# Kernel tuning notes

Measured on AMD Instinct MI355X. Metric: run time of the kernel, lower is better.

Reference implementation:

```python
import jax, jax.numpy as jnp
import numpy as np

D_MODEL = 1024
N_HEADS = 16
D_K = D_MODEL // N_HEADS
D_FF = 4096
EPS = 1e-5


def layer_norm(x, g, b):
    mu = jnp.mean(x, axis=-1, keepdims=True)
    var = jnp.var(x, axis=-1, keepdims=True)
    return (x - mu) * jax.lax.rsqrt(var + EPS) * g + b


def setup_inputs() -> dict:
    key = jax.random.key(0)
    ks = jax.random.split(key, 16)
    B, S = 4, 2048
    s_in = 1.0 / np.sqrt(D_MODEL)
    s_ff = 1.0 / np.sqrt(D_FF)
    return {
        "x": jax.random.normal(ks[0], (B, S, D_MODEL), jnp.float32),
        "mask": jnp.ones((B, 1, 1, S), jnp.int32),
        "Wq": jax.random.normal(ks[1], (D_MODEL, D_MODEL), jnp.float32) * s_in,
        "bq": jnp.zeros((D_MODEL,), jnp.float32),
        "Wk": jax.random.normal(ks[2], (D_MODEL, D_MODEL), jnp.float32) * s_in,
        "bk": jnp.zeros((D_MODEL,), jnp.float32),
        "Wv": jax.random.normal(ks[3], (D_MODEL, D_MODEL), jnp.float32) * s_in,
        "bv": jnp.zeros((D_MODEL,), jnp.float32),
        "Wo": jax.random.normal(ks[4], (D_MODEL, D_MODEL), jnp.float32) * s_in,
        "bo": jnp.zeros((D_MODEL,), jnp.float32),
        "W1": jax.random.normal(ks[5], (D_MODEL, D_FF), jnp.float32) * s_in,
        "b1": jnp.zeros((D_FF,), jnp.float32),
        "W2": jax.random.normal(ks[6], (D_FF, D_MODEL), jnp.float32) * s_ff,
        "b2": jnp.zeros((D_MODEL,), jnp.float32),
        "ln1_g": jnp.ones((D_MODEL,), jnp.float32),
        "ln1_b": jnp.zeros((D_MODEL,), jnp.float32),
        "ln2_g": jnp.ones((D_MODEL,), jnp.float32),
        "ln2_b": jnp.zeros((D_MODEL,), jnp.float32),
    }


def reference(x, mask, Wq, bq, Wk, bk, Wv, bv, Wo, bo, W1, b1, W2, b2,
              ln1_g, ln1_b, ln2_g, ln2_b):
    B, S, _ = x.shape
    h = layer_norm(x, ln1_g, ln1_b)  # norm1(x), used for q/k/v
    # project and split heads: [B,S,D] -> [B,H,S,Dk]
    def heads(t):
        return t.reshape(B, S, N_HEADS, D_K).transpose(0, 2, 1, 3)
    Q = heads(h @ Wq + bq)
    K = heads(h @ Wk + bk)
    V = heads(h @ Wv + bv)
    scores = jnp.einsum('bhqd,bhkd->bhqk', Q, K) / jnp.sqrt(jnp.float32(D_K))
    scores = jnp.where(mask == 0, jnp.float32(-1e9), scores)
    attn = jax.nn.softmax(scores, axis=-1)
    out = jnp.einsum('bhqk,bhkd->bhqd', attn, V)
    out = out.transpose(0, 2, 1, 3).reshape(B, S, D_MODEL)
    attn_out = out @ Wo + bo
    x = x + attn_out
    # FFN with pre-norm (torch nn.GELU default = exact erf gelu)
    h2 = layer_norm(x, ln2_g, ln2_b)
    ff = jax.nn.gelu(h2 @ W1 + b1, approximate=False) @ W2 + b2
    return x + ff
```

## Files before the change

### kernel.cpp

```cpp
#include <hip/hip_runtime.h>
#include <stdint.h>
#include <string.h>


typedef unsigned int       u32;
typedef unsigned short     u16;
typedef __bf16 bf16x8 __attribute__((ext_vector_type(8)));
typedef float  floatx4 __attribute__((ext_vector_type(4)));

#define D_MODEL 1024
#define N_HEADS 16
#define D_K     64
#define D_FF    4096
#define S_LEN   2048
#define N_TOK   8192
#define LDQKV   3072

__device__ __forceinline__ u16 f2b(float f) {
    u32 u = __float_as_uint(f);
    u32 r = (u + 0x7fffu + ((u >> 16) & 1u)) >> 16;
    return (u16)r;
}

__device__ __forceinline__ float fast_gelu(float x) {
    float t = x * x;
    float y = x * 1.5957691216057308f * fmaf(t, 0.044715f, 1.0f);
    return x * __builtin_amdgcn_rcpf(1.0f + __expf(-y));
}

__device__ __forceinline__ void gl_lds16(const void* g, void* l) {
    __builtin_amdgcn_global_load_lds(
        (const __attribute__((address_space(1))) u32*)g,
        (__attribute__((address_space(3))) u32*)l, 16, 0, 0);
}

__global__ __launch_bounds__(256) void transpose_bf16_kernel(
    const float* __restrict__ src, u16* __restrict__ dst, int R, int C)
{
    __shared__ float tile[32][33];
    int cb = blockIdx.x * 32, rb = blockIdx.y * 32;
    int tx = threadIdx.x & 31, ty = threadIdx.x >> 5;
    #pragma unroll
    for (int yy = ty; yy < 32; yy += 8)
        tile[yy][tx] = src[(size_t)(rb + yy) * C + cb + tx];
    __syncthreads();
    #pragma unroll
    for (int yy = ty; yy < 32; yy += 8)
        dst[(size_t)(cb + yy) * R + rb + tx] = f2b(tile[tx][yy]);
}

__global__ __launch_bounds__(256) void ln_kernel(
    const float* __restrict__ x, const float* __restrict__ g,
    const float* __restrict__ b, u16* __restrict__ out)
{
    int row = blockIdx.x;
    int t = threadIdx.x;
    const float4* xr = reinterpret_cast<const float4*>(x + (size_t)row * D_MODEL);
    float4 v = xr[t];
    float s  = v.x + v.y + v.z + v.w;
    float ss = v.x * v.x + v.y * v.y + v.z * v.z + v.w * v.w;
    #pragma unroll
    for (int off = 32; off >= 1; off >>= 1) {
        s  += __shfl_down(s,  off);
        ss += __shfl_down(ss, off);
    }
    __shared__ float red[8];
    int wid = t >> 6, ln = t & 63;
    if (ln == 0) { red[wid] = s; red[4 + wid] = ss; }
    __syncthreads();
    float S  = red[0] + red[1] + red[2] + red[3];
    float SS = red[4] + red[5] + red[6] + red[7];
    float mu  = S * (1.0f / D_MODEL);
    float var = SS * (1.0f / D_MODEL) - mu * mu;
    float rs  = rsqrtf(var + 1e-5f);
    const float4* g4 = reinterpret_cast<const float4*>(g);
    const float4* b4 = reinterpret_cast<const float4*>(b);
    float4 gv = g4[t], bv = b4[t];
    float y0 = (v.x - mu) * rs * gv.x + bv.x;
    float y1 = (v.y - mu) * rs * gv.y + bv.y;
    float y2 = (v.z - mu) * rs * gv.z + bv.z;
    float y3 = (v.w - mu) * rs * gv.w + bv.w;
    uint2 pk;
    pk.x = (u32)f2b(y0) | ((u32)f2b(y1) << 16);
    pk.y = (u32)f2b(y2) | ((u32)f2b(y3) << 16);
    *reinterpret_cast<uint2*>(out + (size_t)row * D_MODEL + t * 4) = pk;
}

template<int MT, int KS>
__global__ __launch_bounds__(256) void gemm_bt(
    const u16* __restrict__ A, const u16* __restrict__ Bt,
    const float* __restrict__ bias, const float* __restrict__ biasK,
    const float* __restrict__ biasV, const float* __restrict__ resid,
    float* __restrict__ outF, u16* __restrict__ outB, u16* __restrict__ outVt,
    int M, int N, int K, int flags)
{
    constexpr int ATILES = MT / 32;
    __shared__ u16 As[MT * 64];
    __shared__ u16 Bs[128 * 64];

    int nbx = N >> 7, nby = M / MT;
    int bid = blockIdx.x;
    int slice = 0;
    if (KS > 1) {
        int nbase = nbx * nby;
        slice = bid / nbase;
        bid  -= slice * nbase;
    }
    int xcd = bid & 7, p = bid >> 3;
    int bandsz = nby >> 3;
    int m0 = (xcd * bandsz + p / nbx) * MT;
    int n0 = (p % nbx) * 128;

    int t = threadIdx.x;
    int wave = t >> 6, lane = t & 63, quad = lane >> 4, lr = lane & 15;
    int wm = (wave >> 1) * (MT / 2), wn = (wave & 1) * 64;

    floatx4 acc[ATILES][4] = {};

    int k0beg = (K / KS) * slice, k0end = k0beg + K / KS;
    for (int k0 = k0beg; k0 < k0end; k0 += 64) {
        #pragma unroll
        for (int i = 0; i < MT / 32; i++) {
            int s = t + i * 256;
            int row = s >> 3, g = ((s & 7) ^ (row & 7)) * 8;
            gl_lds16(&A[(size_t)(m0 + row) * K + k0 + g], &As[s * 8]);
        }
        #pragma unroll
        for (int i = 0; i < 4; i++) {
            int s = t + i * 256;
            int row = s >> 3, g = ((s & 7) ^ (row & 7)) * 8;
            gl_lds16(&Bt[(size_t)(n0 + row) * K + k0 + g], &Bs[s * 8]);
        }
        __syncthreads();

        #pragma unroll
        for (int kk = 0; kk < 2; kk++) {
            bf16x8 af[ATILES], bfr[4];
            #pragma unroll
            for (int mt = 0; mt < ATILES; mt++) {
                int row = wm + mt * 16 + lr;
                int pg = ((kk * 4 + quad) ^ (row & 7)) * 8;
                af[mt] = *reinterpret_cast<const bf16x8*>(&As[row * 64 + pg]);
            }
            #pragma unroll
            for (int nt = 0; nt < 4; nt++) {
                int row = wn + nt * 16 + lr;
                int pg = ((kk * 4 + quad) ^ (row & 7)) * 8;
                bfr[nt] = *reinterpret_cast<const bf16x8*>(&Bs[row * 64 + pg]);
            }
            #pragma unroll
            for (int mt = 0; mt < ATILES; mt++)
                #pragma unroll
                for (int nt = 0; nt < 4; nt++)
                    acc[mt][nt] = __builtin_amdgcn_mfma_f32_16x16x32_bf16(
                        af[mt], bfr[nt], acc[mt][nt], 0, 0, 0);
        }
        __syncthreads();
    }

    bool do_gelu = (flags & 1) != 0;
    #pragma unroll
    for (int mt = 0; mt < ATILES; mt++) {
        #pragma unroll
        for (int nt = 0; nt < 4; nt++) {
            int c = n0 + wn + nt * 16 + lr;
            float bsv;
            if (biasK) {
                if (c >= 2048)      bsv = biasV[c - 2048];
                else if (c >= 1024) bsv = biasK[c - 1024];
                else                bsv = bias[c];
            } else {
                bsv = bias[c];
            }
            if (outVt && c >= 2048) {
                int r0 = m0 + wm + mt * 16 + quad * 4;
                int hb = (c - 2048) >> 6, f = (c - 2048) & 63;
                int bb = r0 >> 11, sIn = r0 & 2047;
                u32 w0 = (u32)f2b(acc[mt][nt][0] + bsv) | ((u32)f2b(acc[mt][nt][1] + bsv) << 16);
                u32 w1 = (u32)f2b(acc[mt][nt][2] + bsv) | ((u32)f2b(acc[mt][nt][3] + bsv) << 16);
                uint2 pk2; pk2.x = w0; pk2.y = w1;
                *reinterpret_cast<uint2*>(
                    &outVt[((size_t)((bb * N_HEADS + hb) * D_K + f)) * S_LEN + sIn]) = pk2;
                continue;
            }
            #pragma unroll
            for (int i = 0; i < 4; i++) {
                int r = m0 + wm + mt * 16 + quad * 4 + i;
                if (KS > 1) {
                    float v = acc[mt][nt][i];
                    if (slice == 0) {
                        v += bsv;
                        if (resid) v += resid[(size_t)r * N + c];
                    }
                    atomicAdd(&outF[(size_t)r * N + c], v);
                    continue;
                }
                float v = acc[mt][nt][i] + bsv;
                if (resid) v += resid[(size_t)r * N + c];
                if (do_gelu) v = fast_gelu(v);
                if (outF) outF[(size_t)r * N + c] = v;
                if (outB) outB[(size_t)r * N + c] = f2b(v);
            }
        }
    }
}

__global__ __launch_bounds__(256, 4) void attn_mfma_kernel(
    const u16* __restrict__ Qkv, const u16* __restrict__ Vt,
    const int* __restrict__ mask, u16* __restrict__ ctx)
{
    __shared__ u16 Ks[64 * 72];
    __shared__ u16 Vs[64 * 72];
    __shared__ u16 Ps[128 * 72];
    __shared__ float Ms[64];

    int b = blockIdx.z, h = blockIdx.y;
    int q0 = blockIdx.x * 128;
    int t = threadIdx.x;
    int wave = t >> 6, lane = t & 63, quad = lane >> 4, lr = lane & 15;
    int wm = wave * 32;

    bf16x8 qf[2][2];
    #pragma unroll
    for (int mt = 0; mt < 2; mt++)
        #pragma unroll
        for (int kk = 0; kk < 2; kk++)
            qf[mt][kk] = *(const bf16x8*)&Qkv[((size_t)(b * S_LEN + q0 + wm + mt * 16 + lr)) * LDQKV
                                              + h * D_K + kk * 32 + quad * 8];

    floatx4 o[2][4] = {};
    float lsum[2] = {0.0f, 0.0f};

    for (int kt = 0; kt < S_LEN / 64; kt++) {
        __syncthreads();
        {
            int row = t >> 2, cg = (t & 3) * 16;
            const u16* kg = &Qkv[((size_t)(b * S_LEN + kt * 64 + row)) * LDQKV + 1024 + h * D_K + cg];
            *(uint4*)&Ks[row * 72 + cg]     = *(const uint4*)kg;
            *(uint4*)&Ks[row * 72 + cg + 8] = *(const uint4*)(kg + 8);
            const u16* vg = &Vt[((size_t)((b * N_HEADS + h) * D_K + row)) * S_LEN + kt * 64 + cg];
            *(uint4*)&Vs[row * 72 + cg]     = *(const uint4*)vg;
            *(uint4*)&Vs[row * 72 + cg + 8] = *(const uint4*)(vg + 8);
            if (t < 64) Ms[t] = (mask[b * S_LEN + kt * 64 + t] == 0) ? -1e30f : 0.0f;
        }
        __syncthreads();

        floatx4 s[2][4] = {};
        {
            bf16x8 bk[2][4];
            #pragma unroll
            for (int kk = 0; kk < 2; kk++)
                #pragma unroll
                for (int n = 0; n < 4; n++)
                    bk[kk][n] = *(const bf16x8*)&Ks[(n * 16 + lr) * 72 + kk * 32 + quad * 8];
            __builtin_amdgcn_s_setprio(1);
            #pragma unroll
            for (int kk = 0; kk < 2; kk++)
                #pragma unroll
                for (int mt = 0; mt < 2; mt++)
                    #pragma unroll
                    for (int n = 0; n < 4; n++)
                        s[mt][n] = __builtin_amdgcn_mfma_f32_16x16x32_bf16(
                            bk[kk][n], qf[mt][kk], s[mt][n], 0, 0, 0);
            __builtin_amdgcn_s_setprio(0);
        }

        #pragma unroll
        for (int mt = 0; mt < 2; mt++) {
            #pragma unroll
            for (int n = 0; n < 4; n++) {
                const float4 mv = *reinterpret_cast<const float4*>(&Ms[n * 16 + quad * 4]);
                float p0 = __expf(fmaf(s[mt][n][0], 0.125f, mv.x));
                float p1 = __expf(fmaf(s[mt][n][1], 0.125f, mv.y));
                float p2 = __expf(fmaf(s[mt][n][2], 0.125f, mv.z));
                float p3 = __expf(fmaf(s[mt][n][3], 0.125f, mv.w));
                lsum[mt] += (p0 + p1) + (p2 + p3);
                u32 w0, w1;
                asm("v_cvt_pk_bf16_f32 %0, %1, %2" : "=v"(w0) : "v"(p0), "v"(p1));
                asm("v_cvt_pk_bf16_f32 %0, %1, %2" : "=v"(w1) : "v"(p2), "v"(p3));
                uint2 pk2; pk2.x = w0; pk2.y = w1;
                *reinterpret_cast<uint2*>(&Ps[(wm + mt * 16 + lr) * 72 + n * 16 + quad * 4]) = pk2;
            }
        }

        bf16x8 bv[4][2];
        #pragma unroll
        for (int kk = 0; kk < 2; kk++)
            #pragma unroll
            for (int n = 0; n < 4; n++)
                bv[n][kk] = *(const bf16x8*)&Vs[(n * 16 + lr) * 72 + kk * 32 + quad * 8];

        __syncthreads();

        __builtin_amdgcn_s_setprio(1);
        #pragma unroll
        for (int kk = 0; kk < 2; kk++) {
            #pragma unroll
            for (int mt = 0; mt < 2; mt++) {
                bf16x8 ap = *(const bf16x8*)&Ps[(wm + mt * 16 + lr) * 72 + kk * 32 + quad * 8];
                #pragma unroll
                for (int n = 0; n < 4; n++)
                    o[mt][n] = __builtin_amdgcn_mfma_f32_16x16x32_bf16(
                        ap, bv[n][kk], o[mt][n], 0, 0, 0);
            }
        }
        __builtin_amdgcn_s_setprio(0);
    }

    float inv[2];
    #pragma unroll
    for (int mt = 0; mt < 2; mt++) {
        float v = lsum[mt];
        v += __shfl_xor(v, 16);
        v += __shfl_xor(v, 32);
        inv[mt] = 1.0f / v;
    }
    #pragma unroll
    for (int mt = 0; mt < 2; mt++) {
        float iv[4];
        #pragma unroll
        for (int i = 0; i < 4; i++) iv[i] = __shfl(inv[mt], quad * 4 + i);
        #pragma unroll
        for (int n = 0; n < 4; n++)
            #pragma unroll
            for (int i = 0; i < 4; i++) {
                int row = q0 + wm + mt * 16 + quad * 4 + i;
                int col = h * D_K + n * 16 + lr;
                ctx[((size_t)(b * S_LEN + row)) * D_MODEL + col] =
                    f2b(o[mt][n][i] * iv[i]);
            }
    }
}

extern "C" void kernel_launch(void* const* d_in, const int* in_sizes, int n_in,
                              void* d_out, int out_size, void* d_ws, size_t ws_size,
                              hipStream_t stream)
{
    const float* x    = (const float*)d_in[0];
    const int*   mask = (const int*)  d_in[1];
    const float* Wq   = (const float*)d_in[2];
    const float* bq   = (const float*)d_in[3];
    const float* Wk   = (const float*)d_in[4];
    const float* bk   = (const float*)d_in[5];
    const float* Wv   = (const float*)d_in[6];
    const float* bv   = (const float*)d_in[7];
    const float* Wo   = (const float*)d_in[8];
    const float* bo   = (const float*)d_in[9];
    const float* W1   = (const float*)d_in[10];
    const float* b1   = (const float*)d_in[11];
    const float* W2   = (const float*)d_in[12];
    const float* b2   = (const float*)d_in[13];
    const float* ln1g = (const float*)d_in[14];
    const float* ln1b = (const float*)d_in[15];
    const float* ln2g = (const float*)d_in[16];
    const float* ln2b = (const float*)d_in[17];
    float* out = (float*)d_out;

    char* ws = (char*)d_ws;
    const size_t MB = 1u << 20;
    u16*   wqkvT = (u16*)(ws + 0 * MB);
    u16*   woT   = (u16*)(ws + 6 * MB);
    u16*   w1T   = (u16*)(ws + 8 * MB);
    u16*   w2T   = (u16*)(ws + 16 * MB);
    u16*   h     = (u16*)(ws + 24 * MB);
    u16*   Qkv   = (u16*)(ws + 40 * MB);
    u16*   ctx   = (u16*)(ws + 88 * MB);
    float* x1    = (float*)(ws + 104 * MB);

    bool full = ws_size >= 216 * MB;
    u16* Vt = full ? (u16*)(ws + 184 * MB) : (u16*)(ws + 104 * MB);
    u16* h2  = full ? (u16*)(ws + 136 * MB) : Qkv;
    u16* ff1 = full ? (u16*)(ws + 152 * MB) : (u16*)(ws + 56 * MB);
    int nchunk = full ? 1 : 2;
    int Mc = N_TOK / nchunk;

    dim3 blk(256);

    transpose_bf16_kernel<<<dim3(32, 32),  blk, 0, stream>>>(Wq, wqkvT,             1024, 1024);
    transpose_bf16_kernel<<<dim3(32, 32),  blk, 0, stream>>>(Wk, wqkvT + 1024*1024, 1024, 1024);
    transpose_bf16_kernel<<<dim3(32, 32),  blk, 0, stream>>>(Wv, wqkvT + 2048*1024, 1024, 1024);
    transpose_bf16_kernel<<<dim3(32, 32),  blk, 0, stream>>>(Wo, woT, 1024, 1024);
    transpose_bf16_kernel<<<dim3(128, 32), blk, 0, stream>>>(W1, w1T, 1024, 4096);
    transpose_bf16_kernel<<<dim3(32, 128), blk, 0, stream>>>(W2, w2T, 4096, 1024);

    ln_kernel<<<N_TOK, blk, 0, stream>>>(x, ln1g, ln1b, h);

    gemm_bt<128,1><<<dim3(24 * 64), blk, 0, stream>>>(h, wqkvT, bq, bk, bv, nullptr,
                                                      nullptr, Qkv, Vt, N_TOK, LDQKV, D_MODEL, 0);

    attn_mfma_kernel<<<dim3(16, 16, 4), blk, 0, stream>>>(Qkv, Vt, mask, ctx);

    gemm_bt<64,1><<<dim3(8 * 128), blk, 0, stream>>>(ctx, woT, bo, nullptr, nullptr, x,
                                                     x1, nullptr, nullptr, N_TOK, D_MODEL, D_MODEL, 0);

    ln_kernel<<<N_TOK, blk, 0, stream>>>(x1, ln2g, ln2b, h2);

    for (int c = 0; c < nchunk; c++) {
        size_t ro = (size_t)c * Mc * D_MODEL;
        size_t rf = (size_t)c * Mc * D_FF;
        gemm_bt<128,1><<<dim3(32 * (Mc / 128)), blk, 0, stream>>>(
            h2 + ro, w1T, b1, nullptr, nullptr, nullptr,
            nullptr, ff1 + (full ? rf : 0), nullptr, Mc, D_FF, D_MODEL, 1);
        gemm_bt<64,2><<<dim3(8 * (Mc / 64) * 2), blk, 0, stream>>>(
            ff1 + (full ? rf : 0), w2T, b2, nullptr, nullptr, x1 + ro,
            out + ro, nullptr, nullptr, Mc, D_MODEL, D_FF, 0);
    }
}
```

Baseline: 628.2 us.

## Swizzle attention LDS tiles, load mask from global, drop split-K for FFN2

```diff
diff --git a/kernel.cpp b/kernel.cpp
--- a/kernel.cpp
+++ b/kernel.cpp
@@ -205,20 +205,20 @@
     }
 }
 
-__global__ __launch_bounds__(256, 4) void attn_mfma_kernel(
+__global__ __launch_bounds__(256, 5) void attn_mfma_kernel(
     const u16* __restrict__ Qkv, const u16* __restrict__ Vt,
     const int* __restrict__ mask, u16* __restrict__ ctx)
 {
-    __shared__ u16 Ks[64 * 72];
-    __shared__ u16 Vs[64 * 72];
-    __shared__ u16 Ps[128 * 72];
-    __shared__ float Ms[64];
+    __shared__ u16 Ks[64 * 64];
+    __shared__ u16 Vs[64 * 64];
+    __shared__ u16 Ps[128 * 64];
 
     int b = blockIdx.z, h = blockIdx.y;
     int q0 = blockIdx.x * 128;
     int t = threadIdx.x;
     int wave = t >> 6, lane = t & 63, quad = lane >> 4, lr = lane & 15;
     int wm = wave * 32;
+    int m7 = lr & 7;
 
     bf16x8 qf[2][2];
     #pragma unroll
@@ -231,19 +231,35 @@
     floatx4 o[2][4] = {};
     float lsum[2] = {0.0f, 0.0f};
 
+    int sr = t >> 2, scg = (t & 3) * 16;
+    int sg0 = (t & 3) * 2;
+    int sp0 = ((sg0)     ^ (sr & 7)) * 8;
+    int sp1 = ((sg0 + 1) ^ (sr & 7)) * 8;
+
     for (int kt = 0; kt < S_LEN / 64; kt++) {
         __syncthreads();
         {
-            int row = t >> 2, cg = (t & 3) * 16;
-            const u16* kg = &Qkv[((size_t)(b * S_LEN + kt * 64 + row)) * LDQKV + 1024 + h * D_K + cg];
-            *(uint4*)&Ks[row * 72 + cg]     = *(const uint4*)kg;
-            *(uint4*)&Ks[row * 72 + cg + 8] = *(const uint4*)(kg + 8);
-            const u16* vg = &Vt[((size_t)((b * N_HEADS + h) * D_K + row)) * S_LEN + kt * 64 + cg];
-            *(uint4*)&Vs[row * 72 + cg]     = *(const uint4*)vg;
-            *(uint4*)&Vs[row * 72 + cg + 8] = *(const uint4*)(vg + 8);
-            if (t < 64) Ms[t] = (mask[b * S_LEN + kt * 64 + t] == 0) ? -1e30f : 0.0f;
+            const u16* kg = &Qkv[((size_t)(b * S_LEN + kt * 64 + sr)) * LDQKV + 1024 + h * D_K + scg];
+            *(uint4*)&Ks[sr * 64 + sp0] = *(const uint4*)kg;
+            *(uint4*)&Ks[sr * 64 + sp1] = *(const uint4*)(kg + 8);
+            const u16* vg = &Vt[((size_t)((b * N_HEADS + h) * D_K + sr)) * S_LEN + kt * 64 + scg];
+            *(uint4*)&Vs[sr * 64 + sp0] = *(const uint4*)vg;
+            *(uint4*)&Vs[sr * 64 + sp1] = *(const uint4*)(vg + 8);
         }
         __syncthreads();
+
+        float4 msk[4];
+        {
+            const int* mrow = &mask[b * S_LEN + kt * 64];
+            #pragma unroll
+            for (int n = 0; n < 4; n++) {
+                int4 mm = *(const int4*)&mrow[n * 16 + quad * 4];
+                msk[n].x = mm.x ? 0.0f : -1e30f;
+                msk[n].y = mm.y ? 0.0f : -1e30f;
+                msk[n].z = mm.z ? 0.0f : -1e30f;
+                msk[n].w = mm.w ? 0.0f : -1e30f;
+            }
+        }
 
         floatx4 s[2][4] = {};
         {
@@ -252,7 +268,7 @@
             for (int kk = 0; kk < 2; kk++)
                 #pragma unroll
                 for (int n = 0; n < 4; n++)
-                    bk[kk][n] = *(const bf16x8*)&Ks[(n * 16 + lr) * 72 + kk * 32 + quad * 8];
+                    bk[kk][n] = *(const bf16x8*)&Ks[(n * 16 + lr) * 64 + ((kk * 4 + quad) ^ m7) * 8];
             __builtin_amdgcn_s_setprio(1);
             #pragma unroll
             for (int kk = 0; kk < 2; kk++)
@@ -269,17 +285,17 @@
         for (int mt = 0; mt < 2; mt++) {
             #pragma unroll
             for (int n = 0; n < 4; n++) {
-                const float4 mv = *reinterpret_cast<const float4*>(&Ms[n * 16 + quad * 4]);
-                float p0 = __expf(fmaf(s[mt][n][0], 0.125f, mv.x));
-                float p1 = __expf(fmaf(s[mt][n][1], 0.125f, mv.y));
-                float p2 = __expf(fmaf(s[mt][n][2], 0.125f, mv.z));
-                float p3 = __expf(fmaf(s[mt][n][3], 0.125f, mv.w));
+                float p0 = __expf(fmaf(s[mt][n][0], 0.125f, msk[n].x));
+                float p1 = __expf(fmaf(s[mt][n][1], 0.125f, msk[n].y));
+                float p2 = __expf(fmaf(s[mt][n][2], 0.125f, msk[n].z));
+                float p3 = __expf(fmaf(s[mt][n][3], 0.125f, msk[n].w));
                 lsum[mt] += (p0 + p1) + (p2 + p3);
                 u32 w0, w1;
                 asm("v_cvt_pk_bf16_f32 %0, %1, %2" : "=v"(w0) : "v"(p0), "v"(p1));
                 asm("v_cvt_pk_bf16_f32 %0, %1, %2" : "=v"(w1) : "v"(p2), "v"(p3));
                 uint2 pk2; pk2.x = w0; pk2.y = w1;
-                *reinterpret_cast<uint2*>(&Ps[(wm + mt * 16 + lr) * 72 + n * 16 + quad * 4]) = pk2;
+                int poff = ((2 * n + (quad >> 1)) ^ m7) * 8 + (quad & 1) * 4;
+                *reinterpret_cast<uint2*>(&Ps[(wm + mt * 16 + lr) * 64 + poff]) = pk2;
             }
         }
 
@@ -288,7 +304,7 @@
         for (int kk = 0; kk < 2; kk++)
             #pragma unroll
             for (int n = 0; n < 4; n++)
-                bv[n][kk] = *(const bf16x8*)&Vs[(n * 16 + lr) * 72 + kk * 32 + quad * 8];
+                bv[n][kk] = *(const bf16x8*)&Vs[(n * 16 + lr) * 64 + ((kk * 4 + quad) ^ m7) * 8];
 
         __syncthreads();
 
@@ -297,7 +313,7 @@
         for (int kk = 0; kk < 2; kk++) {
             #pragma unroll
             for (int mt = 0; mt < 2; mt++) {
-                bf16x8 ap = *(const bf16x8*)&Ps[(wm + mt * 16 + lr) * 72 + kk * 32 + quad * 8];
+                bf16x8 ap = *(const bf16x8*)&Ps[(wm + mt * 16 + lr) * 64 + ((kk * 4 + quad) ^ m7) * 8];
                 #pragma unroll
                 for (int n = 0; n < 4; n++)
                     o[mt][n] = __builtin_amdgcn_mfma_f32_16x16x32_bf16(
@@ -401,7 +417,7 @@
         gemm_bt<128,1><<<dim3(32 * (Mc / 128)), blk, 0, stream>>>(
             h2 + ro, w1T, b1, nullptr, nullptr, nullptr,
             nullptr, ff1 + (full ? rf : 0), nullptr, Mc, D_FF, D_MODEL, 1);
-        gemm_bt<64,2><<<dim3(8 * (Mc / 64) * 2), blk, 0, stream>>>(
+        gemm_bt<64,1><<<dim3(8 * (Mc / 64)), blk, 0, stream>>>(
             ff1 + (full ? rf : 0), w2T, b2, nullptr, nullptr, x1 + ro,
             out + ro, nullptr, nullptr, Mc, D_MODEL, D_FF, 0);
     }
```

Result: slower. 861.7 us (+37.2%).
